# Performance work log

Measured on AMD Instinct MI355X. Metric: run time of the kernel, lower is better.

The kernel has to match this reference:

```python
import jax, jax.numpy as jnp
import numpy as np

B, T, C = 2, 2048, 1024
N_HEAD = 16
HEAD_DIM = C // N_HEAD


def setup_inputs() -> dict:
    key = jax.random.key(0)
    k1, k2, k3 = jax.random.split(key, 3)
    x = jax.random.normal(k1, (B, T, C), dtype=jnp.float32)
    # weights stored as [in, out]; torch Linear computes x @ W.T with weight [out, in]
    W_qkv = jax.random.normal(k2, (C, 3 * C), dtype=jnp.float32) * (1.0 / np.sqrt(C))
    W_proj = jax.random.normal(k3, (C, C), dtype=jnp.float32) * (1.0 / np.sqrt(C))
    return {"x": x, "W_qkv": W_qkv, "W_proj": W_proj}


def reference(x, W_qkv, W_proj):
    Bb, Tt, Cc = x.shape
    qkv = x @ W_qkv                                # [B,T,3C]
    q, k, v = jnp.split(qkv, 3, axis=2)
    # [B,T,H,D] -> [B,H,T,D]
    q = q.reshape(Bb, Tt, N_HEAD, HEAD_DIM).transpose(0, 2, 1, 3)
    k = k.reshape(Bb, Tt, N_HEAD, HEAD_DIM).transpose(0, 2, 1, 3)
    v = v.reshape(Bb, Tt, N_HEAD, HEAD_DIM).transpose(0, 2, 1, 3)
    scale = 1.0 / np.sqrt(HEAD_DIM).astype(np.float32)
    att = jnp.einsum('bhqd,bhkd->bhqk', q, k) * scale   # [B,H,T,T]
    causal = jnp.tril(jnp.ones((Tt, Tt), dtype=bool))
    att = jnp.where(causal[None, None], att, -jnp.inf)
    att = jax.nn.softmax(att, axis=-1)
    y = jnp.einsum('bhqk,bhkd->bhqd', att, v)           # [B,H,T,D]
    y = y.transpose(0, 2, 1, 3).reshape(Bb, Tt, Cc)
    return y @ W_proj
```

## Files before the change

kernel.cpp:

```cpp
#include <hip/hip_runtime.h>
#include <hip/hip_bf16.h>
#include <math.h>


typedef __bf16 bf16_t;
typedef __bf16 bf16x4 __attribute__((ext_vector_type(4)));
typedef __bf16 bf16x8 __attribute__((ext_vector_type(8)));
typedef float  f32x4  __attribute__((ext_vector_type(4)));

#define MFMA16(a, b, c) __builtin_amdgcn_mfma_f32_16x16x32_bf16((a), (b), (c), 0, 0, 0)

#define Bn 2
#define Tn 2048
#define Cn 1024
#define Hn 16
#define Dn 64
#define C3 3072
#define Mn 4096
#define QKW 2048
#define NEG_BIG (-1e30f)
#define SCL2 0.18033688011112042f
#define M2   17.31234049066756f

__device__ __forceinline__ void gload_lds16(const void* g, void* l) {
    __builtin_amdgcn_global_load_lds(
        (const __attribute__((address_space(1))) unsigned int*)g,
        (__attribute__((address_space(3))) unsigned int*)l, 16, 0, 0);
}

__global__ __launch_bounds__(256) void transpose_cvt(const float* __restrict__ in,
                                                     bf16_t* __restrict__ out,
                                                     int K, int N) {
    __shared__ float tile[32][33];
    int n0 = blockIdx.x * 32, k0 = blockIdx.y * 32;
    int tx = threadIdx.x, ty = threadIdx.y;
#pragma unroll
    for (int i = 0; i < 32; i += 8)
        tile[ty + i][tx] = in[(size_t)(k0 + ty + i) * N + n0 + tx];
    __syncthreads();
#pragma unroll
    for (int i = 0; i < 32; i += 8)
        out[(size_t)(n0 + ty + i) * K + k0 + tx] = (bf16_t)tile[tx][ty + i];
}

__global__ __launch_bounds__(256) void cvt_bf16(const float* __restrict__ in,
                                                bf16_t* __restrict__ out) {
    size_t i = ((size_t)blockIdx.x * 256 + threadIdx.x) * 8;
    f32x4 a = *(const f32x4*)(in + i);
    f32x4 b = *(const f32x4*)(in + i + 4);
    bf16x8 r;
    r[0] = (bf16_t)a[0]; r[1] = (bf16_t)a[1]; r[2] = (bf16_t)a[2]; r[3] = (bf16_t)a[3];
    r[4] = (bf16_t)b[0]; r[5] = (bf16_t)b[1]; r[6] = (bf16_t)b[2]; r[7] = (bf16_t)b[3];
    *(bf16x8*)(out + i) = r;
}

template <typename AT, typename CT, int MODE>
__global__ __launch_bounds__(256) void gemm_m97(const AT* __restrict__ A, int lda,
                                                const bf16_t* __restrict__ BT,
                                                CT* __restrict__ Cout, int ldc, int Kd,
                                                bf16_t* __restrict__ qk,
                                                bf16_t* __restrict__ vT) {
    constexpr bool AF32 = (sizeof(AT) == 4);
    __shared__ AT     As[128 * 32];
    __shared__ bf16_t Bs[128 * 32];

    const int tid = threadIdx.x;
    const int w = tid >> 6, lane = tid & 63;
    const int l16 = lane & 15, quad = lane >> 4;
    const int wm = w & 1, wn = w >> 1;
    const int n0 = blockIdx.x * 128;
    const int m0 = blockIdx.y * 128;

    f32x4 zero = {0.f, 0.f, 0.f, 0.f};
    f32x4 acc[4][4];
#pragma unroll
    for (int mb = 0; mb < 4; mb++)
#pragma unroll
        for (int nb = 0; nb < 4; nb++) acc[mb][nb] = zero;

    for (int k = 0; k < Kd; k += 32) {
        __syncthreads();
        if (AF32) {
#pragma unroll
            for (int j = 0; j < 4; j++) {
                int seg = w * 4 + j;
                int r = seg * 8 + (lane >> 3);
                int cc = (lane & 7) ^ (r & 7);
                const float* g = (const float*)A + (size_t)(m0 + r) * lda + k + cc * 4;
                gload_lds16(g, (char*)As + seg * 1024);
            }
        } else {
#pragma unroll
            for (int j = 0; j < 2; j++) {
                int seg = w * 2 + j;
                int r = seg * 16 + (lane >> 2);
                int cc = (lane & 3) ^ (r & 3);
                const bf16_t* g = (const bf16_t*)A + (size_t)(m0 + r) * lda + k + cc * 8;
                gload_lds16(g, (char*)As + seg * 1024);
            }
        }
#pragma unroll
        for (int j = 0; j < 2; j++) {
            int seg = w * 2 + j;
            int r = seg * 16 + (lane >> 2);
            int cc = (lane & 3) ^ (r & 3);
            const bf16_t* g = BT + (size_t)(n0 + r) * Kd + k + cc * 8;
            gload_lds16(g, (char*)Bs + seg * 1024);
        }
        __syncthreads();

        bf16x8 af[4], bf[4];
#pragma unroll
        for (int mb = 0; mb < 4; mb++) {
            int r = wm * 64 + mb * 16 + l16;
            if (AF32) {
                f32x4 x0 = *(const f32x4*)((const char*)As + (r * 8 + ((quad * 2) ^ (r & 7))) * 16);
                f32x4 x1 = *(const f32x4*)((const char*)As + (r * 8 + ((quad * 2 + 1) ^ (r & 7))) * 16);
                bf16x8 t;
                t[0] = (bf16_t)x0[0]; t[1] = (bf16_t)x0[1]; t[2] = (bf16_t)x0[2]; t[3] = (bf16_t)x0[3];
                t[4] = (bf16_t)x1[0]; t[5] = (bf16_t)x1[1]; t[6] = (bf16_t)x1[2]; t[7] = (bf16_t)x1[3];
                af[mb] = t;
            } else {
                af[mb] = *(const bf16x8*)((const char*)As + (r * 4 + (quad ^ (r & 3))) * 16);
            }
        }
#pragma unroll
        for (int nb = 0; nb < 4; nb++) {
            int r = wn * 64 + nb * 16 + l16;
            bf[nb] = *(const bf16x8*)((const char*)Bs + (r * 4 + (quad ^ (r & 3))) * 16);
        }
#pragma unroll
        for (int mb = 0; mb < 4; mb++)
#pragma unroll
            for (int nb = 0; nb < 4; nb++)
                acc[mb][nb] = MFMA16(af[mb], bf[nb], acc[mb][nb]);
    }

#pragma unroll
    for (int mb = 0; mb < 4; mb++)
#pragma unroll
        for (int nb = 0; nb < 4; nb++) {
            const int col = n0 + wn * 64 + nb * 16 + l16;
            const int row0 = m0 + wm * 64 + mb * 16 + quad * 4;
            if (MODE == 0) {
#pragma unroll
                for (int rr = 0; rr < 4; rr++)
                    Cout[(size_t)(row0 + rr) * ldc + col] = (CT)acc[mb][nb][rr];
            } else {
                if (col < 2048) {
#pragma unroll
                    for (int rr = 0; rr < 4; rr++)
                        qk[(size_t)(row0 + rr) * QKW + col] = (bf16_t)acc[mb][nb][rr];
                } else {
                    int hcol = col - 2048;
                    int bb = row0 >> 11, t0 = row0 & 2047;
                    bf16x4 pv;
#pragma unroll
                    for (int rr = 0; rr < 4; rr++) pv[rr] = (bf16_t)acc[mb][nb][rr];
                    *(bf16x4*)(vT + ((size_t)(bb * 1024 + hcol)) * Tn + t0) = pv;
                }
            }
        }
}

__global__ __launch_bounds__(256) void gemm_s(const bf16_t* __restrict__ A, int lda,
                                              const bf16_t* __restrict__ BT,
                                              float* __restrict__ Cout, int ldc, int Kd) {
    __shared__ bf16_t As[64 * 32];
    __shared__ bf16_t Bs[128 * 32];

    const int tid = threadIdx.x;
    const int w = tid >> 6, lane = tid & 63;
    const int l16 = lane & 15, quad = lane >> 4;
    const int wm = w & 1, wn = w >> 1;
    const int n0 = blockIdx.x * 128;
    const int m0 = blockIdx.y * 64;

    f32x4 zero = {0.f, 0.f, 0.f, 0.f};
    f32x4 acc[2][4];
#pragma unroll
    for (int mb = 0; mb < 2; mb++)
#pragma unroll
        for (int nb = 0; nb < 4; nb++) acc[mb][nb] = zero;

    for (int k = 0; k < Kd; k += 32) {
        __syncthreads();
        {
            int r = w * 16 + (lane >> 2);
            int cc = (lane & 3) ^ (r & 3);
            const bf16_t* g = A + (size_t)(m0 + r) * lda + k + cc * 8;
            gload_lds16(g, (char*)As + w * 1024);
        }
#pragma unroll
        for (int j = 0; j < 2; j++) {
            int seg = w * 2 + j;
            int r = seg * 16 + (lane >> 2);
            int cc = (lane & 3) ^ (r & 3);
            const bf16_t* g = BT + (size_t)(n0 + r) * Kd + k + cc * 8;
            gload_lds16(g, (char*)Bs + seg * 1024);
        }
        __syncthreads();

        bf16x8 af[2], bf[4];
#pragma unroll
        for (int mb = 0; mb < 2; mb++) {
            int r = wm * 32 + mb * 16 + l16;
            af[mb] = *(const bf16x8*)((const char*)As + (r * 4 + (quad ^ (r & 3))) * 16);
        }
#pragma unroll
        for (int nb = 0; nb < 4; nb++) {
            int r = wn * 64 + nb * 16 + l16;
            bf[nb] = *(const bf16x8*)((const char*)Bs + (r * 4 + (quad ^ (r & 3))) * 16);
        }
#pragma unroll
        for (int mb = 0; mb < 2; mb++)
#pragma unroll
            for (int nb = 0; nb < 4; nb++)
                acc[mb][nb] = MFMA16(af[mb], bf[nb], acc[mb][nb]);
    }

#pragma unroll
    for (int mb = 0; mb < 2; mb++)
#pragma unroll
        for (int nb = 0; nb < 4; nb++) {
            const int col = n0 + wn * 64 + nb * 16 + l16;
            const int row0 = m0 + wm * 32 + mb * 16 + quad * 4;
#pragma unroll
            for (int rr = 0; rr < 4; rr++)
                Cout[(size_t)(row0 + rr) * ldc + col] = acc[mb][nb][rr];
        }
}

__global__ __launch_bounds__(256) void attn_kernel(bf16_t* __restrict__ qk,
                                                   const bf16_t* __restrict__ vT) {
    const int id = blockIdx.x;
    const int pair = id >> 1;
    const int bh = pair & 31;
    const int xx = pair >> 5;
    const int qt = (id & 1) ? (31 - xx) : xx;
    const int b = bh >> 4, h = bh & 15;

    const int tid = threadIdx.x;
    const int wave = tid >> 6, lane = tid & 63;
    const int l16 = lane & 15, quad = lane >> 4;

    __shared__ bf16_t Kt[64][72];
    __shared__ bf16_t Vt[64][72];
    __shared__ bf16_t Pl[4][16][72];

    bf16_t* qbase = qk + (size_t)b * Tn * QKW + h * Dn;
    const bf16_t* kbase = qk + (size_t)b * Tn * QKW + Cn + h * Dn;
    const bf16_t* vbase = vT + (size_t)(b * 1024 + h * Dn) * Tn;

    const int q0 = qt * 64 + wave * 16;

    bf16x8 qf[2];
#pragma unroll
    for (int ks = 0; ks < 2; ks++)
        qf[ks] = *(const bf16x8*)(qbase + (size_t)(q0 + l16) * QKW + ks * 32 + quad * 8);

    bf16x8 ones;
#pragma unroll
    for (int j = 0; j < 8; j++) ones[j] = (bf16_t)1.0f;

    f32x4 zero = {0.f, 0.f, 0.f, 0.f};
    f32x4 o[4];
    f32x4 ol;
#pragma unroll
    for (int i = 0; i < 4; i++) o[i] = zero;
    ol = zero;

    for (int kb = 0; kb <= qt; kb++) {
        __syncthreads();
        const int key0 = kb * 64;
        for (int c = tid; c < 512; c += 256) {
            int r = c >> 3, col = (c & 7) * 8;
            *(bf16x8*)(&Kt[r][col]) = *(const bf16x8*)(kbase + (size_t)(key0 + r) * QKW + col);
            *(bf16x8*)(&Vt[r][col]) = *(const bf16x8*)(vbase + (size_t)r * Tn + key0 + col);
        }
        __syncthreads();

        f32x4 s[4];
#pragma unroll
        for (int nbk = 0; nbk < 4; nbk++) s[nbk] = zero;
#pragma unroll
        for (int nbk = 0; nbk < 4; nbk++) {
            bf16x8 kf0 = *(const bf16x8*)(&Kt[nbk * 16 + l16][quad * 8]);
            bf16x8 kf1 = *(const bf16x8*)(&Kt[nbk * 16 + l16][32 + quad * 8]);
            s[nbk] = MFMA16(kf0, qf[0], s[nbk]);
            s[nbk] = MFMA16(kf1, qf[1], s[nbk]);
        }

        if (kb == qt) {
            int q = q0 + l16;
#pragma unroll
            for (int nbk = 0; nbk < 4; nbk++)
#pragma unroll
                for (int r = 0; r < 4; r++) {
                    int key = key0 + nbk * 16 + quad * 4 + r;
                    if (key > q) s[nbk][r] = NEG_BIG;
                }
        }

#pragma unroll
        for (int nbk = 0; nbk < 4; nbk++) {
            bf16x4 pk;
#pragma unroll
            for (int r = 0; r < 4; r++)
                pk[r] = (bf16_t)__builtin_exp2f(__builtin_fmaf(s[nbk][r], SCL2, -M2));
            *(bf16x4*)(&Pl[wave][l16][nbk * 16 + quad * 4]) = pk;
        }

#pragma unroll
        for (int ks = 0; ks < 2; ks++) {
            bf16x8 pf = *(const bf16x8*)(&Pl[wave][l16][ks * 32 + quad * 8]);
#pragma unroll
            for (int nbd = 0; nbd < 4; nbd++) {
                bf16x8 vf = *(const bf16x8*)(&Vt[nbd * 16 + l16][ks * 32 + quad * 8]);
                o[nbd] = MFMA16(pf, vf, o[nbd]);
            }
            ol = MFMA16(pf, ones, ol);
        }
    }

#pragma unroll
    for (int nbd = 0; nbd < 4; nbd++)
#pragma unroll
        for (int r = 0; r < 4; r++) {
            int t = q0 + quad * 4 + r;
            float val = o[nbd][r] / ol[r];
            qbase[(size_t)t * QKW + nbd * 16 + l16] = (bf16_t)val;
        }
}

extern "C" void kernel_launch(void* const* d_in, const int* in_sizes, int n_in,
                              void* d_out, int out_size, void* d_ws, size_t ws_size,
                              hipStream_t stream) {
    const float* x     = (const float*)d_in[0];
    const float* Wqkv  = (const float*)d_in[1];
    const float* Wproj = (const float*)d_in[2];
    float* out = (float*)d_out;

    bf16_t* qk     = (bf16_t*)d_ws;
    bf16_t* vT     = qk + (size_t)Mn * QKW;
    bf16_t* wqkvT  = vT + (size_t)QKW * Tn;
    bf16_t* wprojT = wqkvT + (size_t)C3 * Cn;
    bf16_t* xb     = wprojT + (size_t)Cn * Cn;

    const size_t NEED_XB = ((size_t)Mn * QKW + (size_t)QKW * Tn + (size_t)C3 * Cn +
                            (size_t)Cn * Cn + (size_t)Mn * Cn) * sizeof(bf16_t);

    transpose_cvt<<<dim3(C3 / 32, Cn / 32), dim3(32, 8), 0, stream>>>(Wqkv, wqkvT, Cn, C3);
    transpose_cvt<<<dim3(Cn / 32, Cn / 32), dim3(32, 8), 0, stream>>>(Wproj, wprojT, Cn, Cn);

    if (ws_size >= NEED_XB) {
        cvt_bf16<<<dim3((Mn * Cn) / 2048), 256, 0, stream>>>(x, xb);
        gemm_m97<bf16_t, bf16_t, 1><<<dim3(C3 / 128, Mn / 128), 256, 0, stream>>>(
            xb, Cn, wqkvT, (bf16_t*)nullptr, 0, Cn, qk, vT);
    } else {
        gemm_m97<float, bf16_t, 1><<<dim3(C3 / 128, Mn / 128), 256, 0, stream>>>(
            x, Cn, wqkvT, (bf16_t*)nullptr, 0, Cn, qk, vT);
    }
    attn_kernel<<<dim3(1024), 256, 0, stream>>>(qk, vT);
    gemm_s<<<dim3(Cn / 128, Mn / 64), 256, 0, stream>>>(qk, QKW, wprojT, out, Cn, Cn);
}
```

Measured before the change: 198.4 us.

## Double-buffer K/V tiles via async LDS loads and process 128 queries per block

The attention kernel now handles 128-query tiles, with each wave owning 32 rows, so every K/V tile loaded into LDS is reused by twice as many queries. K/V tiles are staged with direct global-to-LDS loads into a swizzled, double-buffered layout, so the next tile is prefetched while the current one is computed, and the second barrier is dropped. The grid is halved to 512 blocks, which reduces occupancy and parallelism and raises register pressure. The causal mask now applies to the last two key tiles.

```diff
diff --git a/kernel.cpp b/kernel.cpp
--- a/kernel.cpp
+++ b/kernel.cpp
@@ -234,103 +234,151 @@
 __global__ __launch_bounds__(256) void attn_kernel(bf16_t* __restrict__ qk,
                                                    const bf16_t* __restrict__ vT) {
     const int id = blockIdx.x;
-    const int pair = id >> 1;
-    const int bh = pair & 31;
-    const int xx = pair >> 5;
-    const int qt = (id & 1) ? (31 - xx) : xx;
+    const int hi = id >> 8;
+    const int idx = id & 255;
+    const int bh = idx & 31;
+    const int xx = idx >> 5;
+    const int qt = hi ? (15 - xx) : xx;
     const int b = bh >> 4, h = bh & 15;
 
     const int tid = threadIdx.x;
     const int wave = tid >> 6, lane = tid & 63;
     const int l16 = lane & 15, quad = lane >> 4;
 
-    __shared__ bf16_t Kt[64][72];
-    __shared__ bf16_t Vt[64][72];
-    __shared__ bf16_t Pl[4][16][72];
+    __shared__ bf16_t Kb[2][64 * 64];
+    __shared__ bf16_t Vb[2][64 * 64];
+    __shared__ bf16_t Pl[4][32][72];
 
     bf16_t* qbase = qk + (size_t)b * Tn * QKW + h * Dn;
     const bf16_t* kbase = qk + (size_t)b * Tn * QKW + Cn + h * Dn;
     const bf16_t* vbase = vT + (size_t)(b * 1024 + h * Dn) * Tn;
 
-    const int q0 = qt * 64 + wave * 16;
-
-    bf16x8 qf[2];
-#pragma unroll
-    for (int ks = 0; ks < 2; ks++)
-        qf[ks] = *(const bf16x8*)(qbase + (size_t)(q0 + l16) * QKW + ks * 32 + quad * 8);
+    const int q0 = qt * 128 + wave * 32;
+
+    bf16x8 qf[2][2];
+#pragma unroll
+    for (int g = 0; g < 2; g++)
+#pragma unroll
+        for (int ks = 0; ks < 2; ks++)
+            qf[g][ks] = *(const bf16x8*)(qbase + (size_t)(q0 + g * 16 + l16) * QKW +
+                                         ks * 32 + quad * 8);
 
     bf16x8 ones;
 #pragma unroll
     for (int j = 0; j < 8; j++) ones[j] = (bf16_t)1.0f;
 
     f32x4 zero = {0.f, 0.f, 0.f, 0.f};
-    f32x4 o[4];
-    f32x4 ol;
-#pragma unroll
-    for (int i = 0; i < 4; i++) o[i] = zero;
-    ol = zero;
-
-    for (int kb = 0; kb <= qt; kb++) {
+    f32x4 o[2][4];
+    f32x4 ol[2];
+#pragma unroll
+    for (int g = 0; g < 2; g++) {
+#pragma unroll
+        for (int i = 0; i < 4; i++) o[g][i] = zero;
+        ol[g] = zero;
+    }
+
+    const int nt = 2 * qt + 2;
+
+    const int r8 = lane >> 3;
+    const int cc = (lane & 7) ^ r8;
+    auto STAGE = [&](int t, int pg) {
+        const int key0 = t * 64;
+#pragma unroll
+        for (int j = 0; j < 2; j++) {
+            int seg = wave * 2 + j;
+            gload_lds16(kbase + (size_t)(key0 + seg * 8 + r8) * QKW + cc * 8,
+                        (char*)&Kb[pg][0] + seg * 1024);
+            gload_lds16(vbase + (size_t)(seg * 8 + r8) * Tn + key0 + cc * 8,
+                        (char*)&Vb[pg][0] + seg * 1024);
+        }
+    };
+
+    STAGE(0, 0);
+    int cur = 0;
+
+    for (int t = 0; t < nt; ++t) {
         __syncthreads();
-        const int key0 = kb * 64;
-        for (int c = tid; c < 512; c += 256) {
-            int r = c >> 3, col = (c & 7) * 8;
-            *(bf16x8*)(&Kt[r][col]) = *(const bf16x8*)(kbase + (size_t)(key0 + r) * QKW + col);
-            *(bf16x8*)(&Vt[r][col]) = *(const bf16x8*)(vbase + (size_t)r * Tn + key0 + col);
-        }
-        __syncthreads();
-
-        f32x4 s[4];
-#pragma unroll
-        for (int nbk = 0; nbk < 4; nbk++) s[nbk] = zero;
-#pragma unroll
-        for (int nbk = 0; nbk < 4; nbk++) {
-            bf16x8 kf0 = *(const bf16x8*)(&Kt[nbk * 16 + l16][quad * 8]);
-            bf16x8 kf1 = *(const bf16x8*)(&Kt[nbk * 16 + l16][32 + quad * 8]);
-            s[nbk] = MFMA16(kf0, qf[0], s[nbk]);
-            s[nbk] = MFMA16(kf1, qf[1], s[nbk]);
-        }
-
-        if (kb == qt) {
-            int q = q0 + l16;
-#pragma unroll
-            for (int nbk = 0; nbk < 4; nbk++)
-#pragma unroll
-                for (int r = 0; r < 4; r++) {
-                    int key = key0 + nbk * 16 + quad * 4 + r;
-                    if (key > q) s[nbk][r] = NEG_BIG;
-                }
-        }
-
-#pragma unroll
-        for (int nbk = 0; nbk < 4; nbk++) {
-            bf16x4 pk;
-#pragma unroll
-            for (int r = 0; r < 4; r++)
-                pk[r] = (bf16_t)__builtin_exp2f(__builtin_fmaf(s[nbk][r], SCL2, -M2));
-            *(bf16x4*)(&Pl[wave][l16][nbk * 16 + quad * 4]) = pk;
-        }
+        if (t + 1 < nt) STAGE(t + 1, cur ^ 1);
+
+        const char* Kc = (const char*)&Kb[cur][0];
+        const char* Vc = (const char*)&Vb[cur][0];
+
+        bf16x8 kf[2][4];
+#pragma unroll
+        for (int ks = 0; ks < 2; ks++)
+#pragma unroll
+            for (int nbk = 0; nbk < 4; nbk++) {
+                int R = nbk * 16 + l16;
+                kf[ks][nbk] = *(const bf16x8*)(Kc + R * 128 +
+                                               (((ks * 4 + quad) ^ (R & 7)) << 4));
+            }
+
+#pragma unroll
+        for (int g = 0; g < 2; g++) {
+            f32x4 s[4];
+#pragma unroll
+            for (int nbk = 0; nbk < 4; nbk++) s[nbk] = zero;
+#pragma unroll
+            for (int nbk = 0; nbk < 4; nbk++) {
+                s[nbk] = MFMA16(kf[0][nbk], qf[g][0], s[nbk]);
+                s[nbk] = MFMA16(kf[1][nbk], qf[g][1], s[nbk]);
+            }
+
+            if (t >= nt - 2) {
+                int q = q0 + g * 16 + l16;
+#pragma unroll
+                for (int nbk = 0; nbk < 4; nbk++)
+#pragma unroll
+                    for (int r = 0; r < 4; r++) {
+                        int key = t * 64 + nbk * 16 + quad * 4 + r;
+                        if (key > q) s[nbk][r] = NEG_BIG;
+                    }
+            }
+
+#pragma unroll
+            for (int nbk = 0; nbk < 4; nbk++) {
+                bf16x4 pk;
+#pragma unroll
+                for (int r = 0; r < 4; r++)
+                    pk[r] = (bf16_t)__builtin_exp2f(__builtin_fmaf(s[nbk][r], SCL2, -M2));
+                *(bf16x4*)(&Pl[wave][g * 16 + l16][nbk * 16 + quad * 4]) = pk;
+            }
+        }
+
+        bf16x8 pf[2][2];
+#pragma unroll
+        for (int g = 0; g < 2; g++)
+#pragma unroll
+            for (int ks = 0; ks < 2; ks++)
+                pf[g][ks] = *(const bf16x8*)(&Pl[wave][g * 16 + l16][ks * 32 + quad * 8]);
 
 #pragma unroll
         for (int ks = 0; ks < 2; ks++) {
-            bf16x8 pf = *(const bf16x8*)(&Pl[wave][l16][ks * 32 + quad * 8]);
 #pragma unroll
             for (int nbd = 0; nbd < 4; nbd++) {
-                bf16x8 vf = *(const bf16x8*)(&Vt[nbd * 16 + l16][ks * 32 + quad * 8]);
-                o[nbd] = MFMA16(pf, vf, o[nbd]);
-            }
-            ol = MFMA16(pf, ones, ol);
-        }
+                int R = nbd * 16 + l16;
+                bf16x8 vf = *(const bf16x8*)(Vc + R * 128 +
+                                             (((ks * 4 + quad) ^ (R & 7)) << 4));
+                o[0][nbd] = MFMA16(pf[0][ks], vf, o[0][nbd]);
+                o[1][nbd] = MFMA16(pf[1][ks], vf, o[1][nbd]);
+            }
+            ol[0] = MFMA16(pf[0][ks], ones, ol[0]);
+            ol[1] = MFMA16(pf[1][ks], ones, ol[1]);
+        }
+
+        cur ^= 1;
     }
 
 #pragma unroll
-    for (int nbd = 0; nbd < 4; nbd++)
-#pragma unroll
-        for (int r = 0; r < 4; r++) {
-            int t = q0 + quad * 4 + r;
-            float val = o[nbd][r] / ol[r];
-            qbase[(size_t)t * QKW + nbd * 16 + l16] = (bf16_t)val;
-        }
+    for (int g = 0; g < 2; g++)
+#pragma unroll
+        for (int nbd = 0; nbd < 4; nbd++)
+#pragma unroll
+            for (int r = 0; r < 4; r++) {
+                int tq = q0 + g * 16 + quad * 4 + r;
+                float val = o[g][nbd][r] / ol[g][r];
+                qbase[(size_t)tq * QKW + nbd * 16 + l16] = (bf16_t)val;
+            }
 }
 
 extern "C" void kernel_launch(void* const* d_in, const int* in_sizes, int n_in,
@@ -361,6 +409,6 @@
         gemm_m97<float, bf16_t, 1><<<dim3(C3 / 128, Mn / 128), 256, 0, stream>>>(
             x, Cn, wqkvT, (bf16_t*)nullptr, 0, Cn, qk, vT);
     }
-    attn_kernel<<<dim3(1024), 256, 0, stream>>>(qk, vT);
+    attn_kernel<<<dim3(512), 256, 0, stream>>>(qk, vT);
     gemm_s<<<dim3(Cn / 128, Mn / 64), 256, 0, stream>>>(qk, QKW, wprojT, out, Cn, Cn);
 }
```

Measured after the change: 194.7 us. No clear change (-1.9%).
